# Optimization experiments

Measured on AMD Instinct MI355X. Metric: run time of the kernel, lower is better.

The kernel has to match this reference:

```python
import jax, jax.numpy as jnp
import numpy as np


def setup_inputs() -> dict:
    key = jax.random.key(0)
    ks = jax.random.split(key, 8)
    B, L, D, H = 4, 2048, 4096, 8
    BW = D // H
    std = 1.0 / np.sqrt(BW)
    x = jax.random.normal(ks[0], (B, L, D), dtype=jnp.float32)
    segment_pos = jax.random.randint(ks[1], (B, L), 0, 1024)
    prev_h = jax.random.normal(ks[2], (B, D), dtype=jnp.float32)
    w_in = jax.random.normal(ks[3], (H, BW, BW), dtype=jnp.float32) * std
    b_in = jnp.zeros((H, BW), dtype=jnp.float32)
    w_a = jax.random.normal(ks[4], (H, BW, BW), dtype=jnp.float32) * std
    b_a = jnp.zeros((H, BW), dtype=jnp.float32)
    # a_param init: uniform on ring [0.9, 0.999], softplus-inverse transform
    unif = jax.random.uniform(ks[5], (D,), dtype=jnp.float32)
    min_rad, max_rad = 0.9, 0.999
    a_real = 0.5 * jnp.log(unif * (max_rad**2 - min_rad**2) + min_rad**2 + 1e-8)
    a_param = jnp.log(jnp.exp(-a_real) - 1.0)
    return {"x": x, "segment_pos": segment_pos, "prev_h": prev_h,
            "w_in": w_in, "b_in": b_in, "w_a": w_a, "b_a": b_a,
            "a_param": a_param}


def _block_diag_linear(x, w, b):
    # x: [B,L,D]; w: [H,BW,BW]; b: [H,BW]
    B, L, D = x.shape
    H = w.shape[0]
    xr = x.reshape(B, L, H, D // H)
    y = jnp.einsum('blhi,hij->blhj', xr, w) + b
    return y.reshape(B, L, D)


def reference(x, segment_pos, prev_h, w_in, b_in, w_a, b_a, a_param):
    # reset indicator at document boundaries (segment_pos == 0)
    reset = (segment_pos == 0).astype(x.dtype)          # [B,L]
    gate_x = jax.nn.sigmoid(_block_diag_linear(x, w_in, b_in))
    gate_a = jax.nn.sigmoid(_block_diag_linear(x, w_a, b_a))
    log_a = -8.0 * gate_a * jax.nn.softplus(a_param)    # [B,L,D]
    a = jnp.exp(log_a)
    multiplier = jnp.sqrt(1.0 - jnp.exp(2.0 * log_a) + 1e-6)
    multiplier = reset[..., None] + (1.0 - reset)[..., None] * multiplier
    normalized_x = x * gate_x * multiplier
    # zero the decay at reset positions (hidden state reset)
    a = a * (1.0 - reset)[..., None]
    # linear recurrence y_t = a_t * y_{t-1} + x_t (initial hidden state = 0,
    # matching the torch L>1 path which does not use prev_h)
    def combine(c1, c2):
        a1, b1 = c1
        a2, b2 = c2
        return (a2 * a1, a2 * b1 + b2)
    _, y = jax.lax.associative_scan(combine, (a, normalized_x), axis=1)
    return y
```

## Files before the change

### kernel.cpp

```cpp
#include <hip/hip_runtime.h>
#include <hip/hip_bf16.h>

typedef _Float16 f16;
typedef _Float16 f16x2 __attribute__((ext_vector_type(2)));
typedef _Float16 f16x4 __attribute__((ext_vector_type(4)));
typedef _Float16 f16x8 __attribute__((ext_vector_type(8)));
typedef float f32x4 __attribute__((ext_vector_type(4)));

#define B_  4
#define L_  2048
#define D_  4096
#define H_  8
#define BW_ 512
#define M_  (B_*L_)
#define CHUNK 128
#define NCH (L_/CHUNK)
#define LOG2E 1.4426950408889634f

static const size_t OFF_WPK   = 0;
static const size_t OFF_MSP   = 8ull<<20;
static const size_t OFF_XH    = 9ull<<20;
static const size_t OFF_YLAP  = 73ull<<20;
static const size_t OFF_SUMA  = 208ull<<20;
static const size_t OFF_SUMY  = 209ull<<20;
static const size_t OFF_CARRY = 210ull<<20;

__device__ __forceinline__ void gl16(const void* g, void* l) {
    __builtin_amdgcn_global_load_lds(
        (const __attribute__((address_space(1))) unsigned int*)g,
        (__attribute__((address_space(3))) unsigned int*)l, 16, 0, 0);
}

__global__ __launch_bounds__(256)
void prep_all(const float* __restrict__ w_in, const float* __restrict__ w_a,
              const float* __restrict__ a_param, const float* __restrict__ x,
              f16* __restrict__ wpk, float* __restrict__ msp2,
              f16* __restrict__ xh) {
    const int bid = blockIdx.x;
    const int tid = threadIdx.x;
    if (bid < 1024) {
        const int kt  = bid & 7;
        const int n32 = (bid >> 3) & 15;
        const int h   = bid >> 7;
        if (bid < 16) {
            int d = bid * 256 + tid;
            float v = a_param[d];
            msp2[d] = -8.f * log1pf(expf(v)) * LOG2E;
        }
#pragma unroll
        for (int q = 0; q < 2; ++q) {
            int slot = q * 256 + tid;
            int lane = slot & 63;
            int fidx = slot >> 6;
            int g    = fidx >> 2;
            int fn   = (fidx >> 1) & 1;
            int kk2  = fidx & 1;
            int row = n32 * 32 + fn * 16 + (lane & 15);
            int col = kt * 64 + kk2 * 32 + ((lane >> 4) << 3);
            const float* src = (g ? w_a : w_in) + (size_t)h * BW_ * BW_;
            f16x8 v;
#pragma unroll
            for (int e = 0; e < 8; ++e)
                v[e] = (f16)src[(size_t)(col + e) * BW_ + row];
            size_t o = ((((size_t)(h * 16 + n32) * 8 + kt) * 8) + fidx) * 64 + lane;
            *(f16x8*)(wpk + o * 8) = v;
        }
    } else {
        size_t i = ((size_t)(bid - 1024) * 256 + tid) * 8;
        const size_t stride = (size_t)2048 * 256 * 8;
        for (; i < (size_t)M_ * D_; i += stride) {
            f32x4 v0 = *(const f32x4*)(x + i);
            f32x4 v1 = *(const f32x4*)(x + i + 4);
            f16x8 hv;
            hv[0] = (f16)v0.x; hv[1] = (f16)v0.y; hv[2] = (f16)v0.z; hv[3] = (f16)v0.w;
            hv[4] = (f16)v1.x; hv[5] = (f16)v1.y; hv[6] = (f16)v1.z; hv[7] = (f16)v1.w;
            *(f16x8*)(xh + i) = hv;
        }
    }
}

#define BM 128
#define BN 64
#define BKK 64
#define NT (BW_/BKK)
#define BUFB 16384

#define SMEM_BYTES 49664

__global__ __launch_bounds__(256, 3)
void gemm_gates(const f16*   __restrict__ xh,
                const int*   __restrict__ segpos,
                const f16*   __restrict__ wpk,
                const float* __restrict__ b_in,
                const float* __restrict__ b_a,
                const float* __restrict__ msp2,
                f16x2* __restrict__ ylap,
                float* __restrict__ sumA,
                float* __restrict__ sumY) {
    __shared__ __align__(16) char smem[SMEM_BYTES];
    f16*   om_s = (f16*)smem;
    f16*   xn_s = (f16*)(smem + 16896);
    float* segA = (float*)(smem + 33792);
    float* segY = (float*)(smem + 34944);
    float* rst_s= (float*)(smem + 49152);

    const int tid  = threadIdx.x;
    const int m0   = blockIdx.x * BM;
    const int n0   = blockIdx.y * BN;
    const int h    = blockIdx.z;
    const int lane = tid & 63;
    const int wid  = tid >> 6;
    const int wr   = wid >> 1;
    const int wc   = wid & 1;

    f32x4 accX[4][2] = {};
    f32x4 accA[4][2] = {};

    if (tid < BM) rst_s[tid] = (segpos[m0 + tid] == 0) ? 1.f : 0.f;

    const int grow  = lane >> 3;
    const int gcolS = (((lane & 7) ^ grow) << 3);
    const f16* aSrc = xh + (size_t)(m0 + wid * 32 + grow) * D_ + h * BW_ + gcolS;

    const f16* wbase = wpk + ((size_t)(h * 16) + (n0 >> 5) + wc) * 32768;

    const int swz  = (lane & 7) << 3;
    const int kx   = (lane >> 4) << 3;
    const int arow = wr * 64 + (lane & 15);
    const int rowb = wr * 64 + ((lane >> 4) << 2);
    const int txo  = (n0 >> 6) + 2;

    f16x8 bfr[2][8];

#define STAGE_A(T)                                                            \
    {                                                                         \
        const int ktg = ((T) + txo) & (NT - 1);                               \
        f16* Asb = (f16*)(smem + ((T) % 3) * BUFB);                           \
        _Pragma("unroll")                                                     \
        for (int q = 0; q < 4; ++q)                                           \
            gl16(aSrc + ktg * BKK + (size_t)q * 8 * D_,                       \
                 &Asb[(wid * 32 + q * 8) * 64]);                              \
    }
#define LOAD_B(T)                                                             \
    {                                                                         \
        const int ktg = ((T) + txo) & (NT - 1);                               \
        const f16* tp = wbase + (size_t)ktg * 4096;                           \
        _Pragma("unroll")                                                     \
        for (int j = 0; j < 8; ++j)                                           \
            bfr[(T) & 1][j] = *(const f16x8*)(tp + j * 512 + lane * 8);       \
    }

    STAGE_A(0);
    LOAD_B(0);
    STAGE_A(1);

#pragma unroll
    for (int t = 0; t < NT; ++t) {
        if (t + 1 < NT) LOAD_B(t + 1);
        if (t + 2 < NT) STAGE_A(t + 2);
        if (t < NT - 2)       asm volatile("s_waitcnt vmcnt(16)" ::: "memory");
        else if (t == NT - 2) asm volatile("s_waitcnt vmcnt(12)" ::: "memory");
        else                  asm volatile("s_waitcnt vmcnt(0)"  ::: "memory");
        __builtin_amdgcn_s_barrier();
        __builtin_amdgcn_sched_barrier(0);

        const f16* Asb = (const f16*)(smem + (t % 3) * BUFB);
#pragma unroll
        for (int kk2 = 0; kk2 < 2; ++kk2) {
            const int kcolS = (kk2 * 32 + kx) ^ swz;
            f16x8 af[4];
#pragma unroll
            for (int fm = 0; fm < 4; ++fm)
                af[fm] = *(const f16x8*)&Asb[(arow + fm * 16) * 64 + kcolS];
#pragma unroll
            for (int fn = 0; fn < 2; ++fn) {
                f16x8 bx = bfr[t & 1][fn * 2 + kk2];
                f16x8 ba = bfr[t & 1][4 + fn * 2 + kk2];
#pragma unroll
                for (int fm = 0; fm < 4; ++fm) {
                    accX[fm][fn] = __builtin_amdgcn_mfma_f32_16x16x32_f16(af[fm], bx, accX[fm][fn], 0, 0, 0);
                    accA[fm][fn] = __builtin_amdgcn_mfma_f32_16x16x32_f16(af[fm], ba, accA[fm][fn], 0, 0, 0);
                }
            }
        }
        __builtin_amdgcn_sched_barrier(0);
        __builtin_amdgcn_s_barrier();
    }
#undef STAGE_A
#undef LOAD_B

    const f16* As1 = (const f16*)smem;
    f16 xvv[2][4][4];
#pragma unroll
    for (int fn = 0; fn < 2; ++fn) {
        const int ctile = wc * 32 + fn * 16 + (lane & 15);
#pragma unroll
        for (int fm = 0; fm < 4; ++fm)
#pragma unroll
            for (int reg = 0; reg < 4; ++reg) {
                const int rowt = rowb + fm * 16 + reg;
                xvv[fn][fm][reg] = As1[rowt * 64 + (ctile ^ ((rowt & 7) << 3))];
            }
    }
    __syncthreads();

    {
#pragma unroll
        for (int fn = 0; fn < 2; ++fn) {
            const int ctile = wc * 32 + fn * 16 + (lane & 15);
            const int d = h * BW_ + n0 + ctile;
            const float bx = b_in[d];
            const float ba = b_a[d];
            const float mspd = msp2[d];
#pragma unroll
            for (int fm = 0; fm < 4; ++fm) {
#pragma unroll
                for (int reg = 0; reg < 4; ++reg) {
                    const int rowt = rowb + fm * 16 + reg;
                    float gxl = accX[fm][fn][reg] + bx;
                    float gal = accA[fm][fn][reg] + ba;
                    float gx = __builtin_amdgcn_rcpf(1.f + __builtin_amdgcn_exp2f(-gxl * LOG2E));
                    float ga = __builtin_amdgcn_rcpf(1.f + __builtin_amdgcn_exp2f(-gal * LOG2E));
                    float a  = __builtin_amdgcn_exp2f(mspd * ga);
                    float a2 = a * a;
                    float mult = __builtin_amdgcn_sqrtf(1.f + 1e-6f - a2);
                    float rv = rst_s[rowt];
                    a *= (1.f - rv);
                    mult = rv + (1.f - rv) * mult;
                    float xv = (float)xvv[fn][fm][reg];
                    om_s[rowt * 66 + ctile] = (f16)(1.f - a);
                    xn_s[rowt * 66 + ctile] = (f16)(xv * gx * mult);
                }
            }
        }
    }
    __syncthreads();

    const int scol = tid & 63;
    const int sseg = tid >> 6;
    {
        float A = 1.f, yv = 0.f;
#pragma unroll 4
        for (int t = sseg * 32; t < sseg * 32 + 32; ++t) {
            float a  = 1.f - (float)om_s[t * 66 + scol];
            float xn = (float)xn_s[t * 66 + scol];
            yv = fmaf(a, yv, xn);
            A *= a;
        }
        segA[sseg * 72 + scol] = A;
        segY[sseg * 72 + scol] = yv;
    }
    __syncthreads();

    {
        float cy = 0.f, pA = 1.f;
        for (int s = 0; s < sseg; ++s) {
            float As_ = segA[s * 72 + scol];
            float Ys_ = segY[s * 72 + scol];
            cy = fmaf(As_, cy, Ys_);
            pA *= As_;
        }
        float Arun = 1.f, yv = cy;
        const size_t obase = (size_t)(m0 + sseg * 32) * D_ + h * BW_ + n0 + scol;
#pragma unroll 4
        for (int i = 0; i < 32; ++i) {
            const int t = sseg * 32 + i;
            float a  = 1.f - (float)om_s[t * 66 + scol];
            float xn = (float)xn_s[t * 66 + scol];
            yv = fmaf(a, yv, xn);
            Arun *= a;
            f16x2 p;
            p[0] = (f16)yv;
            p[1] = (f16)(pA * Arun);
            ylap[obase + (size_t)i * D_] = p;
        }
        if (sseg == 3) {
            const int bb = m0 >> 11;
            const int cc = (m0 & 2047) >> 7;
            size_t si = ((size_t)bb * NCH + cc) * D_ + h * BW_ + n0 + scol;
            sumA[si] = pA * Arun;
            sumY[si] = yv;
        }
    }
}

__global__ __launch_bounds__(256)
void scan_mid(const float* __restrict__ sumA, const float* __restrict__ sumY,
              float* __restrict__ carry) {
    int d = blockIdx.x * 256 + threadIdx.x;
    int b = blockIdx.y;
    float hcur = 0.f;
#pragma unroll
    for (int c = 0; c < NCH; ++c) {
        size_t si = ((size_t)b * NCH + c) * D_ + d;
        carry[si] = hcur;
        hcur = fmaf(sumA[si], hcur, sumY[si]);
    }
}

__global__ __launch_bounds__(256)
void scan_apply(const float* __restrict__ carry, const f16x2* __restrict__ ylap,
                float* __restrict__ y) {
    size_t i4 = (size_t)blockIdx.x * 256 + threadIdx.x;
    const size_t stride = (size_t)gridDim.x * 256;
    const size_t n4 = (size_t)M_ * D_ / 4;
    for (; i4 < n4; i4 += stride) {
        size_t i = i4 * 4;
        size_t row = i >> 12;
        int d = (int)(i & 4095);
        int b = (int)(row >> 11);
        int c = ((int)row & 2047) >> 7;
        const float* cp = carry + (((size_t)(b * NCH + c)) << 12) + d;
        f32x4 cv = *(const f32x4*)cp;
        f16x8 pk = *(const f16x8*)(ylap + i);
        f32x4 o;
        o.x = fmaf(cv.x, (float)pk[1], (float)pk[0]);
        o.y = fmaf(cv.y, (float)pk[3], (float)pk[2]);
        o.z = fmaf(cv.z, (float)pk[5], (float)pk[4]);
        o.w = fmaf(cv.w, (float)pk[7], (float)pk[6]);
        *(f32x4*)(y + i) = o;
    }
}

extern "C" void kernel_launch(void* const* d_in, const int* in_sizes, int n_in,
                              void* d_out, int out_size, void* d_ws, size_t ws_size,
                              hipStream_t stream) {
    const float* x       = (const float*)d_in[0];
    const int*   segpos  = (const int*)d_in[1];
    const float* w_in    = (const float*)d_in[3];
    const float* b_in    = (const float*)d_in[4];
    const float* w_a     = (const float*)d_in[5];
    const float* b_a     = (const float*)d_in[6];
    const float* a_param = (const float*)d_in[7];

    float* y  = (float*)d_out;
    char*  ws = (char*)d_ws;
    f16*   wpk   = (f16*)(ws + OFF_WPK);
    float* msp2  = (float*)(ws + OFF_MSP);
    f16*   xh    = (f16*)(ws + OFF_XH);
    f16x2* ylap  = (f16x2*)(ws + OFF_YLAP);
    float* sumA  = (float*)(ws + OFF_SUMA);
    float* sumY  = (float*)(ws + OFF_SUMY);
    float* carry = (float*)(ws + OFF_CARRY);

    prep_all<<<dim3(3072), 256, 0, stream>>>(w_in, w_a, a_param, x, wpk, msp2, xh);
    gemm_gates<<<dim3(M_ / BM, BW_ / BN, H_), 256, 0, stream>>>(
        xh, segpos, wpk, b_in, b_a, msp2, ylap, sumA, sumY);
    scan_mid<<<dim3(D_ / 256, B_), 256, 0, stream>>>(sumA, sumY, carry);
    scan_apply<<<dim3(4096), 256, 0, stream>>>(carry, ylap, y);
}
```

Before: 213.6 us.

## Widen GEMM N-tile to 128, drop B double-buffer, fuse carry scan into apply

The gate GEMM tile grows from 64 to 128 columns per block, so each xh A tile staged in LDS is reused across twice as many output columns. Occupancy drops from 3 to 2 blocks per CU, and the B-fragment register double-buffer is removed in favour of loading B each iteration. The epilogue packs the decay and normalized-x values as interleaved f16x2 in LDS. The separate scan_mid kernel is removed: scan_apply now recomputes the chunk carry from sumA/sumY per block, saving one launch and the carry buffer at the cost of redundant sequential carry work.

```diff
diff --git a/kernel.cpp b/kernel.cpp
--- a/kernel.cpp
+++ b/kernel.cpp
@@ -23,7 +23,6 @@
 static const size_t OFF_YLAP  = 73ull<<20;
 static const size_t OFF_SUMA  = 208ull<<20;
 static const size_t OFF_SUMY  = 209ull<<20;
-static const size_t OFF_CARRY = 210ull<<20;
 
 __device__ __forceinline__ void gl16(const void* g, void* l) {
     __builtin_amdgcn_global_load_lds(
@@ -80,14 +79,14 @@
 }
 
 #define BM 128
-#define BN 64
+#define BN 128
 #define BKK 64
 #define NT (BW_/BKK)
 #define BUFB 16384
 
-#define SMEM_BYTES 49664
-
-__global__ __launch_bounds__(256, 3)
+#define SMEM_BYTES 72320
+
+__global__ __launch_bounds__(256, 2)
 void gemm_gates(const f16*   __restrict__ xh,
                 const int*   __restrict__ segpos,
                 const f16*   __restrict__ wpk,
@@ -98,11 +97,10 @@
                 float* __restrict__ sumA,
                 float* __restrict__ sumY) {
     __shared__ __align__(16) char smem[SMEM_BYTES];
-    f16*   om_s = (f16*)smem;
-    f16*   xn_s = (f16*)(smem + 16896);
-    float* segA = (float*)(smem + 33792);
-    float* segY = (float*)(smem + 34944);
-    float* rst_s= (float*)(smem + 49152);
+    f16x2* axn  = (f16x2*)smem;
+    float* segA = (float*)(smem + 67584);
+    float* segY = (float*)(smem + 69696);
+    float* rst_s= (float*)(smem + 71808);
 
     const int tid  = threadIdx.x;
     const int m0   = blockIdx.x * BM;
@@ -113,8 +111,8 @@
     const int wr   = wid >> 1;
     const int wc   = wid & 1;
 
-    f32x4 accX[4][2] = {};
-    f32x4 accA[4][2] = {};
+    f32x4 accX[4][4] = {};
+    f32x4 accA[4][4] = {};
 
     if (tid < BM) rst_s[tid] = (segpos[m0 + tid] == 0) ? 1.f : 0.f;
 
@@ -122,15 +120,16 @@
     const int gcolS = (((lane & 7) ^ grow) << 3);
     const f16* aSrc = xh + (size_t)(m0 + wid * 32 + grow) * D_ + h * BW_ + gcolS;
 
-    const f16* wbase = wpk + ((size_t)(h * 16) + (n0 >> 5) + wc) * 32768;
+    const f16* wb0 = wpk + ((size_t)(h * 16) + (n0 >> 5) + wc * 2) * 32768;
+    const f16* wb1 = wb0 + 32768;
 
     const int swz  = (lane & 7) << 3;
     const int kx   = (lane >> 4) << 3;
     const int arow = wr * 64 + (lane & 15);
     const int rowb = wr * 64 + ((lane >> 4) << 2);
-    const int txo  = (n0 >> 6) + 2;
-
-    f16x8 bfr[2][8];
+    const int txo  = ((n0 >> 6) + 2) & (NT - 1);
+
+    f16x8 bfr[16];
 
 #define STAGE_A(T)                                                            \
     {                                                                         \
@@ -144,23 +143,31 @@
 #define LOAD_B(T)                                                             \
     {                                                                         \
         const int ktg = ((T) + txo) & (NT - 1);                               \
-        const f16* tp = wbase + (size_t)ktg * 4096;                           \
         _Pragma("unroll")                                                     \
-        for (int j = 0; j < 8; ++j)                                           \
-            bfr[(T) & 1][j] = *(const f16x8*)(tp + j * 512 + lane * 8);       \
+        for (int fn = 0; fn < 4; ++fn) {                                      \
+            const f16* tp = (fn < 2 ? wb0 : wb1) +                            \
+                ((size_t)ktg * 8 + (fn & 1) * 2) * 512 + lane * 8;            \
+            _Pragma("unroll")                                                 \
+            for (int g = 0; g < 2; ++g)                                       \
+                _Pragma("unroll")                                             \
+                for (int kk2 = 0; kk2 < 2; ++kk2)                             \
+                    bfr[fn * 4 + g * 2 + kk2] =                               \
+                        *(const f16x8*)(tp + (g * 4 + kk2) * 512);            \
+        }                                                                     \
     }
 
     STAGE_A(0);
-    LOAD_B(0);
     STAGE_A(1);
 
 #pragma unroll
     for (int t = 0; t < NT; ++t) {
-        if (t + 1 < NT) LOAD_B(t + 1);
-        if (t + 2 < NT) STAGE_A(t + 2);
-        if (t < NT - 2)       asm volatile("s_waitcnt vmcnt(16)" ::: "memory");
-        else if (t == NT - 2) asm volatile("s_waitcnt vmcnt(12)" ::: "memory");
-        else                  asm volatile("s_waitcnt vmcnt(0)"  ::: "memory");
+        LOAD_B(t);
+        if (t + 2 < NT) {
+            STAGE_A(t + 2);
+            asm volatile("s_waitcnt vmcnt(4)" ::: "memory");
+        } else {
+            asm volatile("s_waitcnt vmcnt(0)" ::: "memory");
+        }
         __builtin_amdgcn_s_barrier();
         __builtin_amdgcn_sched_barrier(0);
 
@@ -173,9 +180,9 @@
             for (int fm = 0; fm < 4; ++fm)
                 af[fm] = *(const f16x8*)&Asb[(arow + fm * 16) * 64 + kcolS];
 #pragma unroll
-            for (int fn = 0; fn < 2; ++fn) {
-                f16x8 bx = bfr[t & 1][fn * 2 + kk2];
-                f16x8 ba = bfr[t & 1][4 + fn * 2 + kk2];
+            for (int fn = 0; fn < 4; ++fn) {
+                f16x8 bx = bfr[fn * 4 + kk2];
+                f16x8 ba = bfr[fn * 4 + 2 + kk2];
 #pragma unroll
                 for (int fm = 0; fm < 4; ++fm) {
                     accX[fm][fn] = __builtin_amdgcn_mfma_f32_16x16x32_f16(af[fm], bx, accX[fm][fn], 0, 0, 0);
@@ -189,25 +196,25 @@
 #undef STAGE_A
 #undef LOAD_B
 
-    const f16* As1 = (const f16*)smem;
-    f16 xvv[2][4][4];
-#pragma unroll
-    for (int fn = 0; fn < 2; ++fn) {
-        const int ctile = wc * 32 + fn * 16 + (lane & 15);
+    const f16* AsL = (const f16*)(smem + wc * BUFB);
+    f16 xvv[4][4][4];
+#pragma unroll
+    for (int fn = 0; fn < 4; ++fn) {
+        const int c5 = fn * 16 + (lane & 15);
 #pragma unroll
         for (int fm = 0; fm < 4; ++fm)
 #pragma unroll
             for (int reg = 0; reg < 4; ++reg) {
                 const int rowt = rowb + fm * 16 + reg;
-                xvv[fn][fm][reg] = As1[rowt * 64 + (ctile ^ ((rowt & 7) << 3))];
+                xvv[fn][fm][reg] = AsL[rowt * 64 + (c5 ^ ((rowt & 7) << 3))];
             }
     }
     __syncthreads();
 
     {
 #pragma unroll
-        for (int fn = 0; fn < 2; ++fn) {
-            const int ctile = wc * 32 + fn * 16 + (lane & 15);
+        for (int fn = 0; fn < 4; ++fn) {
+            const int ctile = wc * 64 + fn * 16 + (lane & 15);
             const int d = h * BW_ + n0 + ctile;
             const float bx = b_in[d];
             const float ba = b_a[d];
@@ -228,56 +235,60 @@
                     a *= (1.f - rv);
                     mult = rv + (1.f - rv) * mult;
                     float xv = (float)xvv[fn][fm][reg];
-                    om_s[rowt * 66 + ctile] = (f16)(1.f - a);
-                    xn_s[rowt * 66 + ctile] = (f16)(xv * gx * mult);
+                    f16x2 p;
+                    p[0] = (f16)(1.f - a);
+                    p[1] = (f16)(xv * gx * mult);
+                    axn[rowt * 132 + ctile] = p;
                 }
             }
         }
     }
     __syncthreads();
 
-    const int scol = tid & 63;
-    const int sseg = tid >> 6;
-    {
+    const int col = tid & 127;
+    const int sg0 = tid >> 7;
+#pragma unroll
+    for (int ss = 0; ss < 2; ++ss) {
+        const int seg = sg0 + ss * 2;
         float A = 1.f, yv = 0.f;
 #pragma unroll 4
-        for (int t = sseg * 32; t < sseg * 32 + 32; ++t) {
-            float a  = 1.f - (float)om_s[t * 66 + scol];
-            float xn = (float)xn_s[t * 66 + scol];
-            yv = fmaf(a, yv, xn);
+        for (int i = 0; i < 32; ++i) {
+            f16x2 v = axn[(seg * 32 + i) * 132 + col];
+            float a  = 1.f - (float)v[0];
+            yv = fmaf(a, yv, (float)v[1]);
             A *= a;
         }
-        segA[sseg * 72 + scol] = A;
-        segY[sseg * 72 + scol] = yv;
+        segA[seg * 132 + col] = A;
+        segY[seg * 132 + col] = yv;
     }
     __syncthreads();
 
-    {
+#pragma unroll
+    for (int ss = 0; ss < 2; ++ss) {
+        const int seg = sg0 + ss * 2;
         float cy = 0.f, pA = 1.f;
-        for (int s = 0; s < sseg; ++s) {
-            float As_ = segA[s * 72 + scol];
-            float Ys_ = segY[s * 72 + scol];
-            cy = fmaf(As_, cy, Ys_);
+        for (int s = 0; s < seg; ++s) {
+            float As_ = segA[s * 132 + col];
+            cy = fmaf(As_, cy, segY[s * 132 + col]);
             pA *= As_;
         }
         float Arun = 1.f, yv = cy;
-        const size_t obase = (size_t)(m0 + sseg * 32) * D_ + h * BW_ + n0 + scol;
+        const size_t obase = (size_t)(m0 + seg * 32) * D_ + h * BW_ + n0 + col;
 #pragma unroll 4
         for (int i = 0; i < 32; ++i) {
-            const int t = sseg * 32 + i;
-            float a  = 1.f - (float)om_s[t * 66 + scol];
-            float xn = (float)xn_s[t * 66 + scol];
-            yv = fmaf(a, yv, xn);
+            f16x2 v = axn[(seg * 32 + i) * 132 + col];
+            float a  = 1.f - (float)v[0];
+            yv = fmaf(a, yv, (float)v[1]);
             Arun *= a;
             f16x2 p;
             p[0] = (f16)yv;
             p[1] = (f16)(pA * Arun);
             ylap[obase + (size_t)i * D_] = p;
         }
-        if (sseg == 3) {
+        if (seg == 3) {
             const int bb = m0 >> 11;
             const int cc = (m0 & 2047) >> 7;
-            size_t si = ((size_t)bb * NCH + cc) * D_ + h * BW_ + n0 + scol;
+            size_t si = ((size_t)bb * NCH + cc) * D_ + h * BW_ + n0 + col;
             sumA[si] = pA * Arun;
             sumY[si] = yv;
         }
@@ -285,40 +296,34 @@
 }
 
 __global__ __launch_bounds__(256)
-void scan_mid(const float* __restrict__ sumA, const float* __restrict__ sumY,
-              float* __restrict__ carry) {
-    int d = blockIdx.x * 256 + threadIdx.x;
-    int b = blockIdx.y;
-    float hcur = 0.f;
-#pragma unroll
-    for (int c = 0; c < NCH; ++c) {
-        size_t si = ((size_t)b * NCH + c) * D_ + d;
-        carry[si] = hcur;
-        hcur = fmaf(sumA[si], hcur, sumY[si]);
-    }
-}
-
-__global__ __launch_bounds__(256)
-void scan_apply(const float* __restrict__ carry, const f16x2* __restrict__ ylap,
-                float* __restrict__ y) {
-    size_t i4 = (size_t)blockIdx.x * 256 + threadIdx.x;
-    const size_t stride = (size_t)gridDim.x * 256;
-    const size_t n4 = (size_t)M_ * D_ / 4;
-    for (; i4 < n4; i4 += stride) {
-        size_t i = i4 * 4;
-        size_t row = i >> 12;
-        int d = (int)(i & 4095);
-        int b = (int)(row >> 11);
-        int c = ((int)row & 2047) >> 7;
-        const float* cp = carry + (((size_t)(b * NCH + c)) << 12) + d;
-        f32x4 cv = *(const f32x4*)cp;
-        f16x8 pk = *(const f16x8*)(ylap + i);
-        f32x4 o;
-        o.x = fmaf(cv.x, (float)pk[1], (float)pk[0]);
-        o.y = fmaf(cv.y, (float)pk[3], (float)pk[2]);
-        o.z = fmaf(cv.z, (float)pk[5], (float)pk[4]);
-        o.w = fmaf(cv.w, (float)pk[7], (float)pk[6]);
-        *(f32x4*)(y + i) = o;
+void scan_apply(const float* __restrict__ sumA, const float* __restrict__ sumY,
+                const f16x2* __restrict__ ylap, float* __restrict__ y) {
+    const int tid = threadIdx.x;
+    const int d4  = (blockIdx.x * 256 + tid) * 4;
+    const int c   = blockIdx.y >> 2;
+    const int tq  = blockIdx.y & 3;
+    const int b   = blockIdx.z;
+    f32x4 h0 = {0.f, 0.f, 0.f, 0.f};
+    for (int cp = 0; cp < c; ++cp) {
+        size_t si = (((size_t)(b * NCH + cp)) << 12) + d4;
+        f32x4 A = *(const f32x4*)(sumA + si);
+        f32x4 Y = *(const f32x4*)(sumY + si);
+        h0.x = fmaf(A.x, h0.x, Y.x);
+        h0.y = fmaf(A.y, h0.y, Y.y);
+        h0.z = fmaf(A.z, h0.z, Y.z);
+        h0.w = fmaf(A.w, h0.w, Y.w);
+    }
+    size_t base = ((size_t)(b * L_ + c * CHUNK + tq * 32)) * D_ + d4;
+#pragma unroll 4
+    for (int i = 0; i < 32; ++i) {
+        size_t o = base + (size_t)i * D_;
+        f16x8 p = *(const f16x8*)(ylap + o);
+        f32x4 ov;
+        ov.x = fmaf(h0.x, (float)p[1], (float)p[0]);
+        ov.y = fmaf(h0.y, (float)p[3], (float)p[2]);
+        ov.z = fmaf(h0.z, (float)p[5], (float)p[4]);
+        ov.w = fmaf(h0.w, (float)p[7], (float)p[6]);
+        *(f32x4*)(y + o) = ov;
     }
 }
 
@@ -341,11 +346,9 @@
     f16x2* ylap  = (f16x2*)(ws + OFF_YLAP);
     float* sumA  = (float*)(ws + OFF_SUMA);
     float* sumY  = (float*)(ws + OFF_SUMY);
-    float* carry = (float*)(ws + OFF_CARRY);
 
     prep_all<<<dim3(3072), 256, 0, stream>>>(w_in, w_a, a_param, x, wpk, msp2, xh);
     gemm_gates<<<dim3(M_ / BM, BW_ / BN, H_), 256, 0, stream>>>(
         xh, segpos, wpk, b_in, b_a, msp2, ylap, sumA, sumY);
-    scan_mid<<<dim3(D_ / 256, B_), 256, 0, stream>>>(sumA, sumY, carry);
-    scan_apply<<<dim3(4096), 256, 0, stream>>>(carry, ylap, y);
-}
+    scan_apply<<<dim3(D_ / 1024, NCH * 4, B_), 256, 0, stream>>>(sumA, sumY, ylap, y);
+}
```

New measurement: 228.6 us. 1.07x slower.

## Fuse chunked scan into GEMM with sequential chunk loop, dropping intermediate buffers

Applied to the files above, without the earlier changes.

Each block now owns a (column tile, head, batch) slice and loops over all sequence chunks, carrying the recurrence state in shared memory. This removes the f16 ylap intermediate and the separate scan_mid and scan_apply kernels, so y is written once in fp32. In exchange, the grid shrinks to 256 blocks at occupancy one with a serialized chunk loop, which reduces parallelism and latency hiding. Precision also improves because the a and xn values stay in fp32 in shared memory.

```diff
diff --git a/kernel.cpp b/kernel.cpp
--- a/kernel.cpp
+++ b/kernel.cpp
@@ -2,9 +2,8 @@
 #include <hip/hip_bf16.h>
 
 typedef _Float16 f16;
-typedef _Float16 f16x2 __attribute__((ext_vector_type(2)));
-typedef _Float16 f16x4 __attribute__((ext_vector_type(4)));
 typedef _Float16 f16x8 __attribute__((ext_vector_type(8)));
+typedef float f32x2 __attribute__((ext_vector_type(2)));
 typedef float f32x4 __attribute__((ext_vector_type(4)));
 
 #define B_  4
@@ -17,13 +16,9 @@
 #define NCH (L_/CHUNK)
 #define LOG2E 1.4426950408889634f
 
-static const size_t OFF_WPK   = 0;
-static const size_t OFF_MSP   = 8ull<<20;
-static const size_t OFF_XH    = 9ull<<20;
-static const size_t OFF_YLAP  = 73ull<<20;
-static const size_t OFF_SUMA  = 208ull<<20;
-static const size_t OFF_SUMY  = 209ull<<20;
-static const size_t OFF_CARRY = 210ull<<20;
+static const size_t OFF_WPK = 0;
+static const size_t OFF_MSP = 8ull<<20;
+static const size_t OFF_XH  = 9ull<<20;
 
 __device__ __forceinline__ void gl16(const void* g, void* l) {
     __builtin_amdgcn_global_load_lds(
@@ -85,42 +80,37 @@
 #define NT (BW_/BKK)
 #define BUFB 16384
 
-#define SMEM_BYTES 49664
-
-__global__ __launch_bounds__(256, 3)
-void gemm_gates(const f16*   __restrict__ xh,
-                const int*   __restrict__ segpos,
-                const f16*   __restrict__ wpk,
-                const float* __restrict__ b_in,
-                const float* __restrict__ b_a,
-                const float* __restrict__ msp2,
-                f16x2* __restrict__ ylap,
-                float* __restrict__ sumA,
-                float* __restrict__ sumY) {
+#define SMEM_BYTES 120064
+
+__global__ __launch_bounds__(256, 1)
+void gemm_scan(const f16*   __restrict__ xh,
+               const int*   __restrict__ segpos,
+               const f16*   __restrict__ wpk,
+               const float* __restrict__ b_in,
+               const float* __restrict__ b_a,
+               const float* __restrict__ msp2,
+               float* __restrict__ y) {
     __shared__ __align__(16) char smem[SMEM_BYTES];
-    f16*   om_s = (f16*)smem;
-    f16*   xn_s = (f16*)(smem + 16896);
-    float* segA = (float*)(smem + 33792);
-    float* segY = (float*)(smem + 34944);
-    float* rst_s= (float*)(smem + 49152);
+    f32x2* axn   = (f32x2*)(smem + 49152);
+    float* segA  = (float*)(smem + 116736);
+    float* segY  = (float*)(smem + 117888);
+    float* rst_s = (float*)(smem + 119040);
+    float* carry = (float*)(smem + 119552);
 
     const int tid  = threadIdx.x;
-    const int m0   = blockIdx.x * BM;
-    const int n0   = blockIdx.y * BN;
-    const int h    = blockIdx.z;
+    const int n0   = blockIdx.x * BN;
+    const int h    = blockIdx.y;
+    const int bb   = blockIdx.z;
     const int lane = tid & 63;
     const int wid  = tid >> 6;
     const int wr   = wid >> 1;
     const int wc   = wid & 1;
 
-    f32x4 accX[4][2] = {};
-    f32x4 accA[4][2] = {};
-
-    if (tid < BM) rst_s[tid] = (segpos[m0 + tid] == 0) ? 1.f : 0.f;
+    if (tid < 64) { carry[tid] = 0.f; carry[64 + tid] = 0.f; }
 
     const int grow  = lane >> 3;
     const int gcolS = (((lane & 7) ^ grow) << 3);
-    const f16* aSrc = xh + (size_t)(m0 + wid * 32 + grow) * D_ + h * BW_ + gcolS;
+    const f16* aBase = xh + (size_t)(bb * L_ + wid * 32 + grow) * D_ + h * BW_ + gcolS;
 
     const f16* wbase = wpk + ((size_t)(h * 16) + (n0 >> 5) + wc) * 32768;
 
@@ -128,83 +118,101 @@
     const int kx   = (lane >> 4) << 3;
     const int arow = wr * 64 + (lane & 15);
     const int rowb = wr * 64 + ((lane >> 4) << 2);
-    const int txo  = (n0 >> 6) + 2;
+    const int txo  = ((n0 >> 6) + 2) & (NT - 1);
+    const int col  = tid & 63;
+    const int seg  = tid >> 6;
 
     f16x8 bfr[2][8];
 
-#define STAGE_A(T)                                                            \
+#define STAGE_A(ASRC, SLOT)                                                   \
     {                                                                         \
-        const int ktg = ((T) + txo) & (NT - 1);                               \
-        f16* Asb = (f16*)(smem + ((T) % 3) * BUFB);                           \
+        const int ktg = ((SLOT) + txo) & (NT - 1);                            \
+        f16* Asb = (f16*)(smem + ((SLOT) % 3) * BUFB);                        \
         _Pragma("unroll")                                                     \
         for (int q = 0; q < 4; ++q)                                           \
-            gl16(aSrc + ktg * BKK + (size_t)q * 8 * D_,                       \
+            gl16((ASRC) + ktg * BKK + (size_t)q * 8 * D_,                     \
                  &Asb[(wid * 32 + q * 8) * 64]);                              \
     }
-#define LOAD_B(T)                                                             \
+#define LOAD_B(SLOT)                                                          \
     {                                                                         \
-        const int ktg = ((T) + txo) & (NT - 1);                               \
+        const int ktg = ((SLOT) + txo) & (NT - 1);                            \
         const f16* tp = wbase + (size_t)ktg * 4096;                           \
         _Pragma("unroll")                                                     \
         for (int j = 0; j < 8; ++j)                                           \
-            bfr[(T) & 1][j] = *(const f16x8*)(tp + j * 512 + lane * 8);       \
+            bfr[(SLOT) & 1][j] = *(const f16x8*)(tp + j * 512 + lane * 8);    \
     }
 
-    STAGE_A(0);
+    STAGE_A(aBase, 0);
+    STAGE_A(aBase, 1);
     LOAD_B(0);
-    STAGE_A(1);
-
-#pragma unroll
-    for (int t = 0; t < NT; ++t) {
-        if (t + 1 < NT) LOAD_B(t + 1);
-        if (t + 2 < NT) STAGE_A(t + 2);
-        if (t < NT - 2)       asm volatile("s_waitcnt vmcnt(16)" ::: "memory");
-        else if (t == NT - 2) asm volatile("s_waitcnt vmcnt(12)" ::: "memory");
-        else                  asm volatile("s_waitcnt vmcnt(0)"  ::: "memory");
-        __builtin_amdgcn_s_barrier();
-        __builtin_amdgcn_sched_barrier(0);
-
-        const f16* Asb = (const f16*)(smem + (t % 3) * BUFB);
-#pragma unroll
-        for (int kk2 = 0; kk2 < 2; ++kk2) {
-            const int kcolS = (kk2 * 32 + kx) ^ swz;
-            f16x8 af[4];
+
+    for (int c = 0; c < NCH; ++c) {
+        const int m0 = bb * L_ + c * CHUNK;
+        const f16* aSrc  = aBase + (size_t)(c * CHUNK) * D_;
+        const f16* aSrcN = aSrc + (size_t)CHUNK * D_;
+
+        if (tid < BM) rst_s[tid] = (segpos[m0 + tid] == 0) ? 1.f : 0.f;
+
+        f32x4 accX[4][2] = {};
+        f32x4 accA[4][2] = {};
+
+#pragma unroll
+        for (int t = 0; t < NT; ++t) {
+            if (t == 0)
+                asm volatile("s_waitcnt vmcnt(0)" ::: "memory");
+            if (t + 1 < NT) LOAD_B(t + 1);
+            if (t + 2 < NT) STAGE_A(aSrc, t + 2);
+            if (t > 0) {
+                if (t < NT - 1) asm volatile("s_waitcnt vmcnt(12)" ::: "memory");
+                else            asm volatile("s_waitcnt vmcnt(0)"  ::: "memory");
+            }
+            __builtin_amdgcn_s_barrier();
+            __builtin_amdgcn_sched_barrier(0);
+
+            const f16* Asb = (const f16*)(smem + (t % 3) * BUFB);
+#pragma unroll
+            for (int kk2 = 0; kk2 < 2; ++kk2) {
+                const int kcolS = (kk2 * 32 + kx) ^ swz;
+                f16x8 af[4];
+#pragma unroll
+                for (int fm = 0; fm < 4; ++fm)
+                    af[fm] = *(const f16x8*)&Asb[(arow + fm * 16) * 64 + kcolS];
+#pragma unroll
+                for (int fn = 0; fn < 2; ++fn) {
+                    f16x8 bx = bfr[t & 1][fn * 2 + kk2];
+                    f16x8 ba = bfr[t & 1][4 + fn * 2 + kk2];
+#pragma unroll
+                    for (int fm = 0; fm < 4; ++fm) {
+                        accX[fm][fn] = __builtin_amdgcn_mfma_f32_16x16x32_f16(af[fm], bx, accX[fm][fn], 0, 0, 0);
+                        accA[fm][fn] = __builtin_amdgcn_mfma_f32_16x16x32_f16(af[fm], ba, accA[fm][fn], 0, 0, 0);
+                    }
+                }
+            }
+            __builtin_amdgcn_sched_barrier(0);
+            __builtin_amdgcn_s_barrier();
+        }
+
+        const f16* AsL = (const f16*)smem;
+        f16 xvv[2][4][4];
+#pragma unroll
+        for (int fn = 0; fn < 2; ++fn) {
+            const int ctile = wc * 32 + fn * 16 + (lane & 15);
 #pragma unroll
             for (int fm = 0; fm < 4; ++fm)
-                af[fm] = *(const f16x8*)&Asb[(arow + fm * 16) * 64 + kcolS];
-#pragma unroll
-            for (int fn = 0; fn < 2; ++fn) {
-                f16x8 bx = bfr[t & 1][fn * 2 + kk2];
-                f16x8 ba = bfr[t & 1][4 + fn * 2 + kk2];
-#pragma unroll
-                for (int fm = 0; fm < 4; ++fm) {
-                    accX[fm][fn] = __builtin_amdgcn_mfma_f32_16x16x32_f16(af[fm], bx, accX[fm][fn], 0, 0, 0);
-                    accA[fm][fn] = __builtin_amdgcn_mfma_f32_16x16x32_f16(af[fm], ba, accA[fm][fn], 0, 0, 0);
+#pragma unroll
+                for (int reg = 0; reg < 4; ++reg) {
+                    const int rowt = rowb + fm * 16 + reg;
+                    xvv[fn][fm][reg] = AsL[rowt * 64 + (ctile ^ ((rowt & 7) << 3))];
                 }
-            }
-        }
-        __builtin_amdgcn_sched_barrier(0);
-        __builtin_amdgcn_s_barrier();
-    }
-#undef STAGE_A
-#undef LOAD_B
-
-    const f16* As1 = (const f16*)smem;
-    f16 xvv[2][4][4];
-#pragma unroll
-    for (int fn = 0; fn < 2; ++fn) {
-        const int ctile = wc * 32 + fn * 16 + (lane & 15);
-#pragma unroll
-        for (int fm = 0; fm < 4; ++fm)
-#pragma unroll
-            for (int reg = 0; reg < 4; ++reg) {
-                const int rowt = rowb + fm * 16 + reg;
-                xvv[fn][fm][reg] = As1[rowt * 64 + (ctile ^ ((rowt & 7) << 3))];
-            }
-    }
-    __syncthreads();
-
-    {
+        }
+        __syncthreads();
+
+        if (c + 1 < NCH) {
+            STAGE_A(aSrcN, 0);
+            STAGE_A(aSrcN, 1);
+            LOAD_B(0);
+        }
+
 #pragma unroll
         for (int fn = 0; fn < 2; ++fn) {
             const int ctile = wc * 32 + fn * 16 + (lane & 15);
@@ -228,98 +236,45 @@
                     a *= (1.f - rv);
                     mult = rv + (1.f - rv) * mult;
                     float xv = (float)xvv[fn][fm][reg];
-                    om_s[rowt * 66 + ctile] = (f16)(1.f - a);
-                    xn_s[rowt * 66 + ctile] = (f16)(xv * gx * mult);
+                    f32x2 p;
+                    p[0] = a;
+                    p[1] = xv * gx * mult;
+                    axn[rowt * 66 + ctile] = p;
                 }
             }
         }
+        __syncthreads();
+
+        {
+            float A = 1.f, yv = 0.f;
+#pragma unroll 4
+            for (int i = 0; i < 32; ++i) {
+                f32x2 v = axn[(seg * 32 + i) * 66 + col];
+                yv = fmaf(v[0], yv, v[1]);
+                A *= v[0];
+            }
+            segA[seg * 72 + col] = A;
+            segY[seg * 72 + col] = yv;
+        }
+        __syncthreads();
+
+        {
+            float yv = carry[(c & 1) * 64 + col];
+            for (int s = 0; s < seg; ++s)
+                yv = fmaf(segA[s * 72 + col], yv, segY[s * 72 + col]);
+            const size_t obase = (size_t)(m0 + seg * 32) * D_ + h * BW_ + n0 + col;
+#pragma unroll 4
+            for (int i = 0; i < 32; ++i) {
+                f32x2 v = axn[(seg * 32 + i) * 66 + col];
+                yv = fmaf(v[0], yv, v[1]);
+                y[obase + (size_t)i * D_] = yv;
+            }
+            if (seg == 3)
+                carry[((c + 1) & 1) * 64 + col] = yv;
+        }
     }
-    __syncthreads();
-
-    const int scol = tid & 63;
-    const int sseg = tid >> 6;
-    {
-        float A = 1.f, yv = 0.f;
-#pragma unroll 4
-        for (int t = sseg * 32; t < sseg * 32 + 32; ++t) {
-            float a  = 1.f - (float)om_s[t * 66 + scol];
-            float xn = (float)xn_s[t * 66 + scol];
-            yv = fmaf(a, yv, xn);
-            A *= a;
-        }
-        segA[sseg * 72 + scol] = A;
-        segY[sseg * 72 + scol] = yv;
-    }
-    __syncthreads();
-
-    {
-        float cy = 0.f, pA = 1.f;
-        for (int s = 0; s < sseg; ++s) {
-            float As_ = segA[s * 72 + scol];
-            float Ys_ = segY[s * 72 + scol];
-            cy = fmaf(As_, cy, Ys_);
-            pA *= As_;
-        }
-        float Arun = 1.f, yv = cy;
-        const size_t obase = (size_t)(m0 + sseg * 32) * D_ + h * BW_ + n0 + scol;
-#pragma unroll 4
-        for (int i = 0; i < 32; ++i) {
-            const int t = sseg * 32 + i;
-            float a  = 1.f - (float)om_s[t * 66 + scol];
-            float xn = (float)xn_s[t * 66 + scol];
-            yv = fmaf(a, yv, xn);
-            Arun *= a;
-            f16x2 p;
-            p[0] = (f16)yv;
-            p[1] = (f16)(pA * Arun);
-            ylap[obase + (size_t)i * D_] = p;
-        }
-        if (sseg == 3) {
-            const int bb = m0 >> 11;
-            const int cc = (m0 & 2047) >> 7;
-            size_t si = ((size_t)bb * NCH + cc) * D_ + h * BW_ + n0 + scol;
-            sumA[si] = pA * Arun;
-            sumY[si] = yv;
-        }
-    }
-}
-
-__global__ __launch_bounds__(256)
-void scan_mid(const float* __restrict__ sumA, const float* __restrict__ sumY,
-              float* __restrict__ carry) {
-    int d = blockIdx.x * 256 + threadIdx.x;
-    int b = blockIdx.y;
-    float hcur = 0.f;
-#pragma unroll
-    for (int c = 0; c < NCH; ++c) {
-        size_t si = ((size_t)b * NCH + c) * D_ + d;
-        carry[si] = hcur;
-        hcur = fmaf(sumA[si], hcur, sumY[si]);
-    }
-}
-
-__global__ __launch_bounds__(256)
-void scan_apply(const float* __restrict__ carry, const f16x2* __restrict__ ylap,
-                float* __restrict__ y) {
-    size_t i4 = (size_t)blockIdx.x * 256 + threadIdx.x;
-    const size_t stride = (size_t)gridDim.x * 256;
-    const size_t n4 = (size_t)M_ * D_ / 4;
-    for (; i4 < n4; i4 += stride) {
-        size_t i = i4 * 4;
-        size_t row = i >> 12;
-        int d = (int)(i & 4095);
-        int b = (int)(row >> 11);
-        int c = ((int)row & 2047) >> 7;
-        const float* cp = carry + (((size_t)(b * NCH + c)) << 12) + d;
-        f32x4 cv = *(const f32x4*)cp;
-        f16x8 pk = *(const f16x8*)(ylap + i);
-        f32x4 o;
-        o.x = fmaf(cv.x, (float)pk[1], (float)pk[0]);
-        o.y = fmaf(cv.y, (float)pk[3], (float)pk[2]);
-        o.z = fmaf(cv.z, (float)pk[5], (float)pk[4]);
-        o.w = fmaf(cv.w, (float)pk[7], (float)pk[6]);
-        *(f32x4*)(y + i) = o;
-    }
+#undef STAGE_A
+#undef LOAD_B
 }
 
 extern "C" void kernel_launch(void* const* d_in, const int* in_sizes, int n_in,
@@ -335,17 +290,11 @@
 
     float* y  = (float*)d_out;
     char*  ws = (char*)d_ws;
-    f16*   wpk   = (f16*)(ws + OFF_WPK);
-    float* msp2  = (float*)(ws + OFF_MSP);
-    f16*   xh    = (f16*)(ws + OFF_XH);
-    f16x2* ylap  = (f16x2*)(ws + OFF_YLAP);
-    float* sumA  = (float*)(ws + OFF_SUMA);
-    float* sumY  = (float*)(ws + OFF_SUMY);
-    float* carry = (float*)(ws + OFF_CARRY);
+    f16*   wpk  = (f16*)(ws + OFF_WPK);
+    float* msp2 = (float*)(ws + OFF_MSP);
+    f16*   xh   = (f16*)(ws + OFF_XH);
 
     prep_all<<<dim3(3072), 256, 0, stream>>>(w_in, w_a, a_param, x, wpk, msp2, xh);
-    gemm_gates<<<dim3(M_ / BM, BW_ / BN, H_), 256, 0, stream>>>(
-        xh, segpos, wpk, b_in, b_a, msp2, ylap, sumA, sumY);
-    scan_mid<<<dim3(D_ / 256, B_), 256, 0, stream>>>(sumA, sumY, carry);
-    scan_apply<<<dim3(4096), 256, 0, stream>>>(carry, ylap, y);
+    gemm_scan<<<dim3(BW_ / BN, H_, B_), 256, 0, stream>>>(
+        xh, segpos, wpk, b_in, b_a, msp2, y);
 }
```

New measurement: 219.3 us (median of 2 runs). 2.6% more time.
